# Performance work log

Hardware: AMD Instinct MI355X
Metric: run time of the kernel (lower is better)

## Reference

```python
import jax, jax.numpy as jnp
import numpy as np

B, I, J = 2, 2048, 2048
DIM = 1024
H = 16
DH = 64
INNER = H * DH
EPS = 1e-5


def _layernorm(x, g, b):
    mu = jnp.mean(x, axis=-1, keepdims=True)
    var = jnp.var(x, axis=-1, keepdims=True)
    return (x - mu) * jax.lax.rsqrt(var + EPS) * g + b


def setup_inputs() -> dict:
    key = jax.random.key(0)
    ks = jax.random.split(key, 12)
    s_in = 1.0 / np.sqrt(DIM)
    s_inner = 1.0 / np.sqrt(INNER)
    s_h = 1.0 / np.sqrt(H)
    return {
        "x": jax.random.normal(ks[0], (B, I, DIM), jnp.float32),
        "context": jax.random.normal(ks[1], (B, J, DIM), jnp.float32),
        "ln_g": jnp.ones((DIM,), jnp.float32),
        "ln_b": jnp.zeros((DIM,), jnp.float32),
        "ctx_ln_g": jnp.ones((DIM,), jnp.float32),
        "ctx_ln_b": jnp.zeros((DIM,), jnp.float32),
        "W_qk": jax.random.normal(ks[2], (DIM, INNER), jnp.float32) * s_in,
        "W_ctx_qk": jax.random.normal(ks[3], (DIM, INNER), jnp.float32) * s_in,
        "W_v": jax.random.normal(ks[4], (DIM, INNER), jnp.float32) * s_in,
        "W_ctx_v": jax.random.normal(ks[5], (DIM, INNER), jnp.float32) * s_in,
        "W_out": jax.random.normal(ks[6], (INNER, DIM), jnp.float32) * s_inner,
        "b_out": jnp.zeros((DIM,), jnp.float32),
        "W_ctx_out": jax.random.normal(ks[7], (INNER, DIM), jnp.float32) * s_inner,
        "b_ctx_out": jnp.zeros((DIM,), jnp.float32),
        "th_w": jax.random.normal(ks[8], (H, H), jnp.float32) * s_h,
        "ctx_th_w": jax.random.normal(ks[9], (H, H), jnp.float32) * s_h,
    }


def reference(x, context, ln_g, ln_b, ctx_ln_g, ctx_ln_b, W_qk, W_ctx_qk,
              W_v, W_ctx_v, W_out, b_out, W_ctx_out, b_ctx_out, th_w, ctx_th_w):
    b, i, j = x.shape[0], x.shape[1], context.shape[1]
    scale = DH ** -0.5
    xn = _layernorm(x, ln_g, ln_b)
    cn = _layernorm(context, ctx_ln_g, ctx_ln_b)

    def split_heads(t):  # [b, n, h*d] -> [b, h, n, d]
        return t.reshape(t.shape[0], t.shape[1], H, DH).transpose(0, 2, 1, 3)

    qk = split_heads(xn @ W_qk)            # [b, h, i, d]
    ctx_qk = split_heads(cn @ W_ctx_qk)    # [b, h, j, d]
    v = split_heads(xn @ W_v)              # [b, h, i, d]
    ctx_v = split_heads(cn @ W_ctx_v)      # [b, h, j, d]

    sim = jnp.einsum('bhid,bhjd->bhij', qk, ctx_qk) * scale  # shared sim matrix
    attn = jax.nn.softmax(sim, axis=-1)       # softmax over j
    ctx_attn = jax.nn.softmax(sim, axis=-2)   # softmax over i

    # talking heads: 1x1 conv over head dim
    attn = jnp.einsum('gh,bhij->bgij', th_w, attn)
    ctx_attn = jnp.einsum('gh,bhij->bgij', ctx_th_w, ctx_attn)

    out = jnp.einsum('bhij,bhjd->bhid', attn, ctx_v)       # [b, h, i, d]
    ctx_out = jnp.einsum('bhij,bhid->bhjd', ctx_attn, v)   # [b, h, j, d]

    def merge_heads(t):  # [b, h, n, d] -> [b, n, h*d]
        return t.transpose(0, 2, 1, 3).reshape(t.shape[0], t.shape[2], INNER)

    out = merge_heads(out) @ W_out + b_out
    ctx_out = merge_heads(ctx_out) @ W_ctx_out + b_ctx_out
    return out, ctx_out
```

## Files before the change

kernel.cpp:

```cpp
#include <hip/hip_runtime.h>
#include <hip/hip_bf16.h>
#include <cstdint>

#define DIM_   1024
#define H_     16
#define DH_    64
#define INNER_ 1024
#define B_     2
#define I_     2048
#define J_     2048
#define SCALE_ 0.125f

using bf16x8 = __attribute__((ext_vector_type(8))) short;
using f32x4  = __attribute__((ext_vector_type(4))) float;

__device__ __forceinline__ unsigned short f2bf(float f) {
  unsigned int u = __float_as_uint(f);
  u = (u + 0x7FFFu + ((u >> 16) & 1u)) >> 16;
  return (unsigned short)u;
}
__device__ __forceinline__ float bf2f(unsigned short h) {
  return __uint_as_float(((unsigned int)h) << 16);
}

__device__ __forceinline__ void gld16(const unsigned short* g, unsigned short* l) {
  __builtin_amdgcn_global_load_lds(
      (const __attribute__((address_space(1))) unsigned int*)g,
      (__attribute__((address_space(3))) unsigned int*)l, 16, 0, 0);
}

__global__ __launch_bounds__(256) void ln_cast_kernel(
    const float* __restrict__ in, const float* __restrict__ g,
    const float* __restrict__ bb, unsigned short* __restrict__ out) {
  int row = blockIdx.x;
  int t = threadIdx.x;
  const float4* rp = (const float4*)(in + (size_t)row * DIM_);
  float4 v = rp[t];
  float s  = v.x + v.y + v.z + v.w;
  float ss = v.x * v.x + v.y * v.y + v.z * v.z + v.w * v.w;
  for (int o = 1; o < 64; o <<= 1) {
    s  += __shfl_xor(s, o, 64);
    ss += __shfl_xor(ss, o, 64);
  }
  __shared__ float ls[4], lss[4];
  int wave = t >> 6, lane = t & 63;
  if (lane == 0) { ls[wave] = s; lss[wave] = ss; }
  __syncthreads();
  s  = ls[0] + ls[1] + ls[2] + ls[3];
  ss = lss[0] + lss[1] + lss[2] + lss[3];
  float mu  = s * (1.0f / DIM_);
  float var = ss * (1.0f / DIM_) - mu * mu;
  float rstd = rsqrtf(var + 1e-5f);
  float4 gv = ((const float4*)g)[t];
  float4 bv = ((const float4*)bb)[t];
  ushort4 o4;
  o4.x = f2bf((v.x - mu) * rstd * gv.x + bv.x);
  o4.y = f2bf((v.y - mu) * rstd * gv.y + bv.y);
  o4.z = f2bf((v.z - mu) * rstd * gv.z + bv.z);
  o4.w = f2bf((v.w - mu) * rstd * gv.w + bv.w);
  ((ushort4*)(out + (size_t)row * DIM_))[t] = o4;
}

__global__ __launch_bounds__(256) void transpose_cast_f32(
    const float* __restrict__ in, unsigned short* __restrict__ out, int R, int C) {
  __shared__ float tile[32][33];
  int z = blockIdx.z;
  const float* ip = in + (size_t)z * R * C;
  unsigned short* op = out + (size_t)z * R * C;
  int c0 = blockIdx.x * 32, r0 = blockIdx.y * 32;
  int tx = threadIdx.x, ty = threadIdx.y;
  for (int k = 0; k < 4; k++)
    tile[ty * 4 + k][tx] = ip[(size_t)(r0 + ty * 4 + k) * C + c0 + tx];
  __syncthreads();
  for (int k = 0; k < 4; k++)
    op[(size_t)(c0 + ty * 4 + k) * R + r0 + tx] = f2bf(tile[tx][ty * 4 + k]);
}

__global__ __launch_bounds__(256) void transpose_bf16(
    const unsigned short* __restrict__ in, unsigned short* __restrict__ out, int R, int C) {
  __shared__ unsigned short tile[32][33];
  int z = blockIdx.z;
  const unsigned short* ip = in + (size_t)z * R * C;
  unsigned short* op = out + (size_t)z * R * C;
  int c0 = blockIdx.x * 32, r0 = blockIdx.y * 32;
  int tx = threadIdx.x, ty = threadIdx.y;
  for (int k = 0; k < 4; k++)
    tile[ty * 4 + k][tx] = ip[(size_t)(r0 + ty * 4 + k) * C + c0 + tx];
  __syncthreads();
  for (int k = 0; k < 4; k++)
    op[(size_t)(c0 + ty * 4 + k) * R + r0 + tx] = tile[tx][ty * 4 + k];
}

__global__ __launch_bounds__(256) void gemm_qkv(
    const unsigned short* __restrict__ A0, const unsigned short* __restrict__ A1,
    const unsigned short* __restrict__ Bt0, const unsigned short* __restrict__ Bt1,
    unsigned short* __restrict__ qkO0, unsigned short* __restrict__ vO0,
    unsigned short* __restrict__ qkO1, unsigned short* __restrict__ vO1,
    int M, int K) {
  __shared__ unsigned short As[128 * 32];
  __shared__ unsigned short Bs[128 * 32];
  int z = blockIdx.z;
  const unsigned short* A  = z ? A1 : A0;
  const unsigned short* Bt = z ? Bt1 : Bt0;
  unsigned short* qkO = z ? qkO1 : qkO0;
  unsigned short* vO  = z ? vO1 : vO0;
  int t = threadIdx.x;
  int lane = t & 63, wave = t >> 6;
  int m0 = blockIdx.y * 128, n0 = blockIdx.x * 128;
  int wm = (wave >> 1) * 64, wn = (wave & 1) * 64;
  int l15 = lane & 15, lk = lane >> 4;
  int srow = t >> 2, scol = (t & 3) * 8;
  f32x4 acc[4][4] = {};

  for (int k0 = 0; k0 < K; k0 += 32) {
    gld16(&A[(size_t)(m0 + srow) * K + k0 + scol],       &As[wave * 512]);
    gld16(&A[(size_t)(m0 + srow + 64) * K + k0 + scol],  &As[2048 + wave * 512]);
    gld16(&Bt[(size_t)(n0 + srow) * K + k0 + scol],      &Bs[wave * 512]);
    gld16(&Bt[(size_t)(n0 + srow + 64) * K + k0 + scol], &Bs[2048 + wave * 512]);
    __syncthreads();
    bf16x8 af[4], bfr[4];
#pragma unroll
    for (int mi = 0; mi < 4; mi++) af[mi]  = *(const bf16x8*)&As[(wm + mi * 16 + l15) * 32 + lk * 8];
#pragma unroll
    for (int ni = 0; ni < 4; ni++) bfr[ni] = *(const bf16x8*)&Bs[(wn + ni * 16 + l15) * 32 + lk * 8];
#pragma unroll
    for (int mi = 0; mi < 4; mi++)
#pragma unroll
      for (int ni = 0; ni < 4; ni++)
        acc[mi][ni] = __builtin_amdgcn_mfma_f32_16x16x32_bf16(af[mi], bfr[ni], acc[mi][ni], 0, 0, 0);
    __syncthreads();
  }
  unsigned short* dst = (n0 < 1024) ? qkO : vO;
  int nbase = n0 & 1023;
#pragma unroll
  for (int mi = 0; mi < 4; mi++)
#pragma unroll
    for (int ni = 0; ni < 4; ni++) {
      int col = nbase + wn + ni * 16 + l15;
#pragma unroll
      for (int r = 0; r < 4; r++) {
        int row = m0 + wm + mi * 16 + lk * 4 + r;
        dst[(size_t)row * INNER_ + col] = f2bf(acc[mi][ni][r]);
      }
    }
}

__global__ __launch_bounds__(256) void gemm_out(
    const unsigned short* __restrict__ A0, const unsigned short* __restrict__ A1,
    const unsigned short* __restrict__ Bt0, const unsigned short* __restrict__ Bt1,
    const float* __restrict__ bias0, const float* __restrict__ bias1,
    float* __restrict__ C0, float* __restrict__ C1,
    int M, int N, int K) {
  __shared__ unsigned short As[128 * 32];
  __shared__ unsigned short Bs[128 * 32];
  int z = blockIdx.z;
  const unsigned short* A  = z ? A1 : A0;
  const unsigned short* Bt = z ? Bt1 : Bt0;
  const float* bias = z ? bias1 : bias0;
  float* Cout = z ? C1 : C0;
  int t = threadIdx.x;
  int lane = t & 63, wave = t >> 6;
  int m0 = blockIdx.y * 128, n0 = blockIdx.x * 128;
  int wm = (wave >> 1) * 64, wn = (wave & 1) * 64;
  int l15 = lane & 15, lk = lane >> 4;
  int srow = t >> 2, scol = (t & 3) * 8;
  f32x4 acc[4][4] = {};

  for (int k0 = 0; k0 < K; k0 += 32) {
    gld16(&A[(size_t)(m0 + srow) * K + k0 + scol],       &As[wave * 512]);
    gld16(&A[(size_t)(m0 + srow + 64) * K + k0 + scol],  &As[2048 + wave * 512]);
    gld16(&Bt[(size_t)(n0 + srow) * K + k0 + scol],      &Bs[wave * 512]);
    gld16(&Bt[(size_t)(n0 + srow + 64) * K + k0 + scol], &Bs[2048 + wave * 512]);
    __syncthreads();
    bf16x8 af[4], bfr[4];
#pragma unroll
    for (int mi = 0; mi < 4; mi++) af[mi]  = *(const bf16x8*)&As[(wm + mi * 16 + l15) * 32 + lk * 8];
#pragma unroll
    for (int ni = 0; ni < 4; ni++) bfr[ni] = *(const bf16x8*)&Bs[(wn + ni * 16 + l15) * 32 + lk * 8];
#pragma unroll
    for (int mi = 0; mi < 4; mi++)
#pragma unroll
      for (int ni = 0; ni < 4; ni++)
        acc[mi][ni] = __builtin_amdgcn_mfma_f32_16x16x32_bf16(af[mi], bfr[ni], acc[mi][ni], 0, 0, 0);
    __syncthreads();
  }
#pragma unroll
  for (int mi = 0; mi < 4; mi++)
#pragma unroll
    for (int ni = 0; ni < 4; ni++) {
      int col = n0 + wn + ni * 16 + l15;
      float bsv = bias[col];
#pragma unroll
      for (int r = 0; r < 4; r++) {
        int row = m0 + wm + mi * 16 + lk * 4 + r;
        Cout[(size_t)row * N + col] = acc[mi][ni][r] + bsv;
      }
    }
}

__global__ __launch_bounds__(256) void stats_kernel(
    const unsigned short* __restrict__ qk, const unsigned short* __restrict__ ck,
    float* __restrict__ rsum, float* __restrict__ csum, int NQ, int NK) {
  int zz = blockIdx.z;
  int b = zz & 1, dir = zz >> 1;
  const unsigned short* Q  = dir ? ck : qk;
  const unsigned short* Kc = dir ? qk : ck;
  float* out = dir ? csum : rsum;
  int h = blockIdx.y, i0 = blockIdx.x * 64;
  int t = threadIdx.x, lane = t & 63, wave = t >> 6;
  int l15 = lane & 15, lk = lane >> 4;
  const size_t qbase = ((size_t)b * NQ + i0) * INNER_ + h * DH_;
  bf16x8 af[4][2];
#pragma unroll
  for (int mi = 0; mi < 4; mi++)
#pragma unroll
    for (int ks = 0; ks < 2; ks++)
      af[mi][ks] = *(const bf16x8*)&Q[qbase + (size_t)(mi * 16 + l15) * INNER_ + ks * 32 + lk * 8];
  float racc[4][4] = {};
  for (int j0 = wave * 16; j0 < NK; j0 += 64) {
    const size_t kbase = ((size_t)b * NK + j0 + l15) * INNER_ + h * DH_ + lk * 8;
    bf16x8 b0 = *(const bf16x8*)&Kc[kbase];
    bf16x8 b1 = *(const bf16x8*)&Kc[kbase + 32];
#pragma unroll
    for (int mi = 0; mi < 4; mi++) {
      f32x4 acc = {};
      acc = __builtin_amdgcn_mfma_f32_16x16x32_bf16(af[mi][0], b0, acc, 0, 0, 0);
      acc = __builtin_amdgcn_mfma_f32_16x16x32_bf16(af[mi][1], b1, acc, 0, 0, 0);
#pragma unroll
      for (int r = 0; r < 4; r++) racc[mi][r] += __expf(acc[r] * SCALE_);
    }
  }
#pragma unroll
  for (int o = 1; o < 16; o <<= 1)
#pragma unroll
    for (int mi = 0; mi < 4; mi++)
#pragma unroll
      for (int r = 0; r < 4; r++) racc[mi][r] += __shfl_xor(racc[mi][r], o, 64);
  __shared__ float part[4][64];
  if (l15 == 0)
#pragma unroll
    for (int mi = 0; mi < 4; mi++)
#pragma unroll
      for (int r = 0; r < 4; r++) part[wave][mi * 16 + lk * 4 + r] = racc[mi][r];
  __syncthreads();
  if (t < 64)
    out[((size_t)b * H_ + h) * NQ + i0 + t] = part[0][t] + part[1][t] + part[2][t] + part[3][t];
}

#define MSROW 40
#define MSG   (32 * MSROW + 8)
__global__ __launch_bounds__(256, 2) void fused_attn_kernel(
    const unsigned short* __restrict__ Q, const unsigned short* __restrict__ Kc,
    const unsigned short* __restrict__ Vt, const float* __restrict__ rsum,
    const float* __restrict__ thw,
    float* __restrict__ p0, float* __restrict__ p1,
    float* __restrict__ p2, float* __restrict__ p3,
    int NQ, int NK, int CHUNK) {
  __shared__ unsigned short Pb[4 * 256 * 16];
  __shared__ unsigned short Ms[16 * MSG];
  __shared__ float lrS[512];
  int n = blockIdx.x;
  int combo = n & 7;
  int b = combo >> 2, jc = combo & 3;
  int i0 = (n >> 3) * 32;
  float* __restrict__ Op = (jc == 0) ? p0 : (jc == 1) ? p1 : (jc == 2) ? p2 : p3;
  int t = threadIdx.x, lane = t & 63, wave = t >> 6;
  int l15 = lane & 15, lk = lane >> 4;

  lrS[t]       = -__logf(rsum[((size_t)b * H_ + (t >> 5)) * NQ + i0 + (t & 31)]);
  lrS[t + 256] = -__logf(rsum[((size_t)b * H_ + ((t + 256) >> 5)) * NQ + i0 + (t & 31)]);

  bf16x8 tfrag;
  {
    int part = lk >> 1, hb = (lk & 1) * 8;
#pragma unroll
    for (int e = 0; e < 8; e++) {
      float a = thw[l15 * H_ + hb + e];
      unsigned short hi = f2bf(a);
      tfrag[e] = (short)(part == 0 ? hi : f2bf(a - bf2f(hi)));
    }
  }
  __syncthreads();

  bf16x8 qpre[4][2][2];
#pragma unroll
  for (int hh = 0; hh < 4; hh++)
#pragma unroll
    for (int is = 0; is < 2; is++)
#pragma unroll
      for (int kk = 0; kk < 2; kk++)
        qpre[hh][is][kk] = *(const bf16x8*)&Q[((size_t)b * NQ + i0 + is * 16 + l15) * INNER_
                                              + (wave * 4 + hh) * 64 + kk * 32 + lk * 8];

  f32x4 acc[32] = {};
  const int jbeg = jc * CHUNK;

  for (int js = 0; js < CHUNK; js += 32) {
    int j0 = jbeg + js;
    const unsigned short* Kb0 = Kc + ((size_t)b * NK + j0 + l15) * INNER_;
    const unsigned short* Kb1 = Kb0 + (size_t)16 * INNER_;
    unsigned int stage[2][2][4][2];
#pragma unroll
    for (int hh = 0; hh < 4; hh++) {
      int h = wave * 4 + hh;
      bf16x8 kb00 = *(const bf16x8*)&Kb0[h * 64 + lk * 8];
      bf16x8 kb01 = *(const bf16x8*)&Kb0[h * 64 + 32 + lk * 8];
      bf16x8 kb10 = *(const bf16x8*)&Kb1[h * 64 + lk * 8];
      bf16x8 kb11 = *(const bf16x8*)&Kb1[h * 64 + 32 + lk * 8];
#pragma unroll
      for (int is = 0; is < 2; is++) {
        f32x4 s0 = {}, s1 = {};
        s0 = __builtin_amdgcn_mfma_f32_16x16x32_bf16(qpre[hh][is][0], kb00, s0, 0, 0, 0);
        s0 = __builtin_amdgcn_mfma_f32_16x16x32_bf16(qpre[hh][is][1], kb01, s0, 0, 0, 0);
        s1 = __builtin_amdgcn_mfma_f32_16x16x32_bf16(qpre[hh][is][0], kb10, s1, 0, 0, 0);
        s1 = __builtin_amdgcn_mfma_f32_16x16x32_bf16(qpre[hh][is][1], kb11, s1, 0, 0, 0);
        f32x4 lr = *(const f32x4*)&lrS[h * 32 + is * 16 + lk * 4];
#pragma unroll
        for (int r = 0; r < 4; r++) {
          unsigned int b0 = f2bf(__expf(fmaf(s0[r], SCALE_, lr[r])));
          unsigned int b1 = f2bf(__expf(fmaf(s1[r], SCALE_, lr[r])));
          if (hh & 1) { stage[is][0][r][hh >> 1] |= b0 << 16; stage[is][1][r][hh >> 1] |= b1 << 16; }
          else        { stage[is][0][r][hh >> 1]  = b0;       stage[is][1][r][hh >> 1]  = b1; }
        }
      }
    }
#pragma unroll
    for (int is = 0; is < 2; is++)
#pragma unroll
      for (int jp = 0; jp < 2; jp++)
#pragma unroll
        for (int r = 0; r < 4; r++) {
          int row = (lk * 4 + r) * 16 + l15;
          int col = (wave * 4) ^ ((row & 1) << 3);
          uint2 u = { stage[is][jp][r][0], stage[is][jp][r][1] };
          *(uint2*)&Pb[(is + jp * 2) * 256 * 16 + row * 16 + col] = u;
        }
    __syncthreads();
    {
      int isub = wave & 1, jstrip = wave >> 1;
      const unsigned short* pr = &Pb[(isub + jstrip * 2) * 256 * 16];
#pragma unroll
      for (int p = 0; p < 16; p++) {
        int row = p * 16 + l15;
        int col = ((lk & 1) << 3) ^ ((row & 1) << 3);
        bf16x8 af = *(const bf16x8*)&pr[row * 16 + col];
        f32x4 m = {};
        m = __builtin_amdgcn_mfma_f32_16x16x32_bf16(af, tfrag, m, 0, 0, 0);
        ushort4 o;
        o.x = f2bf(m[0]); o.y = f2bf(m[1]); o.z = f2bf(m[2]); o.w = f2bf(m[3]);
        *(ushort4*)&Ms[l15 * MSG + (isub * 16 + p) * MSROW + jstrip * 16 + lk * 4] = o;
      }
    }
    __syncthreads();
#pragma unroll
    for (int gi = 0; gi < 4; gi++) {
      int g = wave * 4 + gi;
      bf16x8 ma0 = *(const bf16x8*)&Ms[g * MSG + l15 * MSROW + lk * 8];
      bf16x8 ma1 = *(const bf16x8*)&Ms[g * MSG + (16 + l15) * MSROW + lk * 8];
#pragma unroll
      for (int nt = 0; nt < 4; nt++) {
        const size_t vb = ((size_t)b * INNER_ + g * 64 + nt * 16 + l15) * NK + j0 + lk * 8;
        bf16x8 v0 = *(const bf16x8*)&Vt[vb];
        acc[gi * 8 + nt]     = __builtin_amdgcn_mfma_f32_16x16x32_bf16(ma0, v0, acc[gi * 8 + nt], 0, 0, 0);
        acc[gi * 8 + 4 + nt] = __builtin_amdgcn_mfma_f32_16x16x32_bf16(ma1, v0, acc[gi * 8 + 4 + nt], 0, 0, 0);
      }
    }
  }
#pragma unroll
  for (int gi = 0; gi < 4; gi++)
#pragma unroll
    for (int is = 0; is < 2; is++)
#pragma unroll
      for (int nt = 0; nt < 4; nt++) {
        int col = (wave * 4 + gi) * 64 + nt * 16 + l15;
#pragma unroll
        for (int r = 0; r < 4; r++)
          Op[((size_t)b * NQ + i0 + is * 16 + lk * 4 + r) * INNER_ + col] = acc[gi * 8 + is * 4 + nt][r];
      }
}

__global__ __launch_bounds__(256) void reduce_cast_kernel(
    const float* __restrict__ p0, const float* __restrict__ p1,
    const float* __restrict__ p2, const float* __restrict__ p3,
    unsigned short* __restrict__ out, int n4) {
  int idx = blockIdx.x * 256 + threadIdx.x;
  if (idx >= n4) return;
  float4 v = ((const float4*)p0)[idx];
  float4 w = ((const float4*)p1)[idx];
  float4 a = ((const float4*)p2)[idx];
  float4 c = ((const float4*)p3)[idx];
  v.x += w.x + a.x + c.x; v.y += w.y + a.y + c.y;
  v.z += w.z + a.z + c.z; v.w += w.w + a.w + c.w;
  ushort4 o;
  o.x = f2bf(v.x); o.y = f2bf(v.y); o.z = f2bf(v.z); o.w = f2bf(v.w);
  ((ushort4*)out)[idx] = o;
}

extern "C" void kernel_launch(void* const* d_in, const int* in_sizes, int n_in,
                              void* d_out, int out_size, void* d_ws, size_t ws_size,
                              hipStream_t stream) {
  const float* x      = (const float*)d_in[0];
  const float* ctx    = (const float*)d_in[1];
  const float* ln_g   = (const float*)d_in[2];
  const float* ln_b   = (const float*)d_in[3];
  const float* cln_g  = (const float*)d_in[4];
  const float* cln_b  = (const float*)d_in[5];
  const float* W_qk   = (const float*)d_in[6];
  const float* W_cqk  = (const float*)d_in[7];
  const float* W_v    = (const float*)d_in[8];
  const float* W_cv   = (const float*)d_in[9];
  const float* W_out  = (const float*)d_in[10];
  const float* b_out  = (const float*)d_in[11];
  const float* W_cout = (const float*)d_in[12];
  const float* b_cout = (const float*)d_in[13];
  const float* th_w   = (const float*)d_in[14];
  const float* cth_w  = (const float*)d_in[15];

  char* w = (char*)d_ws;
  const size_t SZ_ROW = (size_t)B_ * I_ * DIM_ * 2;
  const size_t SZ_W   = (size_t)DIM_ * INNER_ * 2;
  unsigned short* xn    = (unsigned short*)w; w += SZ_ROW;
  unsigned short* cn    = (unsigned short*)w; w += SZ_ROW;
  unsigned short* WqvX  = (unsigned short*)w; w += 2 * SZ_W;
  unsigned short* WqvC  = (unsigned short*)w; w += 2 * SZ_W;
  unsigned short* Woutt = (unsigned short*)w; w += SZ_W;
  unsigned short* Wcoutt= (unsigned short*)w; w += SZ_W;
  unsigned short* qk    = (unsigned short*)w; w += SZ_ROW;
  unsigned short* ck    = (unsigned short*)w; w += SZ_ROW;
  unsigned short* vv    = (unsigned short*)w; w += SZ_ROW;
  unsigned short* cv    = (unsigned short*)w; w += SZ_ROW;
  unsigned short* vT    = (unsigned short*)w; w += SZ_ROW;
  unsigned short* cvT   = (unsigned short*)w; w += SZ_ROW;
  float* rsum = (float*)w; w += (size_t)B_ * H_ * I_ * 4;
  float* csum = (float*)w; w += (size_t)B_ * H_ * J_ * 4;
  unsigned short* Oh1 = (unsigned short*)w; w += SZ_ROW;
  unsigned short* Oh2 = (unsigned short*)w; w += SZ_ROW;

  const size_t PART = (size_t)B_ * I_ * INNER_ * 4;
  float* p0 = (float*)xn;
  float* p1 = (float*)vv;
  float* p2 = (float*)w;
  float* p3 = (float*)(w + PART);

  dim3 tb(32, 8);
  ln_cast_kernel<<<B_ * I_, 256, 0, stream>>>(x, ln_g, ln_b, xn);
  ln_cast_kernel<<<B_ * J_, 256, 0, stream>>>(ctx, cln_g, cln_b, cn);

  const size_t WOFF = (size_t)DIM_ * INNER_;
  transpose_cast_f32<<<dim3(32, 32, 1), tb, 0, stream>>>(W_qk,   WqvX,        DIM_, INNER_);
  transpose_cast_f32<<<dim3(32, 32, 1), tb, 0, stream>>>(W_v,    WqvX + WOFF, DIM_, INNER_);
  transpose_cast_f32<<<dim3(32, 32, 1), tb, 0, stream>>>(W_cqk,  WqvC,        DIM_, INNER_);
  transpose_cast_f32<<<dim3(32, 32, 1), tb, 0, stream>>>(W_cv,   WqvC + WOFF, DIM_, INNER_);
  transpose_cast_f32<<<dim3(32, 32, 1), tb, 0, stream>>>(W_out,  Woutt, INNER_, DIM_);
  transpose_cast_f32<<<dim3(32, 32, 1), tb, 0, stream>>>(W_cout, Wcoutt,INNER_, DIM_);

  gemm_qkv<<<dim3(2 * INNER_ / 128, (B_ * I_) / 128, 2), 256, 0, stream>>>(
      xn, cn, WqvX, WqvC, qk, vv, ck, cv, B_ * I_, DIM_);

  transpose_bf16<<<dim3(INNER_ / 32, I_ / 32, B_), tb, 0, stream>>>(vv, vT, I_, INNER_);
  transpose_bf16<<<dim3(INNER_ / 32, J_ / 32, B_), tb, 0, stream>>>(cv, cvT, J_, INNER_);

  stats_kernel<<<dim3(I_ / 64, H_, 4), 256, 0, stream>>>(qk, ck, rsum, csum, I_, J_);

  const int n4 = (B_ * I_ * INNER_) / 4;
  fused_attn_kernel<<<(I_ / 32) * 4 * B_, 256, 0, stream>>>(
      qk, ck, cvT, rsum, th_w, p0, p1, p2, p3, I_, J_, J_ / 4);
  reduce_cast_kernel<<<n4 / 256, 256, 0, stream>>>(p0, p1, p2, p3, Oh1, n4);
  fused_attn_kernel<<<(J_ / 32) * 4 * B_, 256, 0, stream>>>(
      ck, qk, vT, csum, cth_w, p0, p1, p2, p3, J_, I_, I_ / 4);
  reduce_cast_kernel<<<n4 / 256, 256, 0, stream>>>(p0, p1, p2, p3, Oh2, n4);

  gemm_out<<<dim3(DIM_ / 128, (B_ * I_) / 128, 2), 256, 0, stream>>>(
      Oh1, Oh2, Woutt, Wcoutt, b_out, b_cout,
      (float*)d_out, ((float*)d_out) + (size_t)B_ * I_ * DIM_,
      B_ * I_, DIM_, INNER_);
}
```

Measured before the change: 782.2 us.

## Split fused attention across eight waves with two heads each

The fused attention kernel now launches with 512 threads (eight waves), and each wave handles two heads instead of four. This halves per-wave accumulators and Q fragments, which reduces register pressure and should allow more waves in flight. The second head's Q fragments are loaded inside the loop instead of held in registers, and the LDS P buffer uses a new XOR swizzle with 32-bit stores and loads. In exchange the kernel issues more LDS transactions and reloads Q each iteration, and more waves contend at each barrier.

```diff
diff --git a/kernel.cpp b/kernel.cpp
--- a/kernel.cpp
+++ b/kernel.cpp
@@ -249,7 +249,7 @@
 
 #define MSROW 40
 #define MSG   (32 * MSROW + 8)
-__global__ __launch_bounds__(256, 2) void fused_attn_kernel(
+__global__ __launch_bounds__(512, 4) void fused_attn_kernel(
     const unsigned short* __restrict__ Q, const unsigned short* __restrict__ Kc,
     const unsigned short* __restrict__ Vt, const float* __restrict__ rsum,
     const float* __restrict__ thw,
@@ -267,8 +267,7 @@
   int t = threadIdx.x, lane = t & 63, wave = t >> 6;
   int l15 = lane & 15, lk = lane >> 4;
 
-  lrS[t]       = -__logf(rsum[((size_t)b * H_ + (t >> 5)) * NQ + i0 + (t & 31)]);
-  lrS[t + 256] = -__logf(rsum[((size_t)b * H_ + ((t + 256) >> 5)) * NQ + i0 + (t & 31)]);
+  lrS[t] = -__logf(rsum[((size_t)b * H_ + (t >> 5)) * NQ + i0 + (t & 31)]);
 
   bf16x8 tfrag;
   {
@@ -282,45 +281,56 @@
   }
   __syncthreads();
 
-  bf16x8 qpre[4][2][2];
-#pragma unroll
-  for (int hh = 0; hh < 4; hh++)
-#pragma unroll
-    for (int is = 0; is < 2; is++)
-#pragma unroll
-      for (int kk = 0; kk < 2; kk++)
-        qpre[hh][is][kk] = *(const bf16x8*)&Q[((size_t)b * NQ + i0 + is * 16 + l15) * INNER_
-                                              + (wave * 4 + hh) * 64 + kk * 32 + lk * 8];
-
-  f32x4 acc[32] = {};
+  const unsigned short* Qrow = Q + ((size_t)b * NQ + i0 + l15) * INNER_;
+  bf16x8 qpre[2][2];
+#pragma unroll
+  for (int is = 0; is < 2; is++)
+#pragma unroll
+    for (int kk = 0; kk < 2; kk++)
+      qpre[is][kk] = *(const bf16x8*)&Qrow[(size_t)(is * 16) * INNER_
+                                           + (wave * 2) * 64 + kk * 32 + lk * 8];
+
+  int xsw2 = (((l15 >> 2) & 3) << 1) | (lk & 1);
+  int colw = (wave * 2) ^ (xsw2 << 1);
+
+  f32x4 acc[16] = {};
   const int jbeg = jc * CHUNK;
 
   for (int js = 0; js < CHUNK; js += 32) {
     int j0 = jbeg + js;
     const unsigned short* Kb0 = Kc + ((size_t)b * NK + j0 + l15) * INNER_;
-    const unsigned short* Kb1 = Kb0 + (size_t)16 * INNER_;
-    unsigned int stage[2][2][4][2];
-#pragma unroll
-    for (int hh = 0; hh < 4; hh++) {
-      int h = wave * 4 + hh;
-      bf16x8 kb00 = *(const bf16x8*)&Kb0[h * 64 + lk * 8];
-      bf16x8 kb01 = *(const bf16x8*)&Kb0[h * 64 + 32 + lk * 8];
-      bf16x8 kb10 = *(const bf16x8*)&Kb1[h * 64 + lk * 8];
-      bf16x8 kb11 = *(const bf16x8*)&Kb1[h * 64 + 32 + lk * 8];
-#pragma unroll
-      for (int is = 0; is < 2; is++) {
-        f32x4 s0 = {}, s1 = {};
-        s0 = __builtin_amdgcn_mfma_f32_16x16x32_bf16(qpre[hh][is][0], kb00, s0, 0, 0, 0);
-        s0 = __builtin_amdgcn_mfma_f32_16x16x32_bf16(qpre[hh][is][1], kb01, s0, 0, 0, 0);
-        s1 = __builtin_amdgcn_mfma_f32_16x16x32_bf16(qpre[hh][is][0], kb10, s1, 0, 0, 0);
-        s1 = __builtin_amdgcn_mfma_f32_16x16x32_bf16(qpre[hh][is][1], kb11, s1, 0, 0, 0);
-        f32x4 lr = *(const f32x4*)&lrS[h * 32 + is * 16 + lk * 4];
-#pragma unroll
-        for (int r = 0; r < 4; r++) {
-          unsigned int b0 = f2bf(__expf(fmaf(s0[r], SCALE_, lr[r])));
-          unsigned int b1 = f2bf(__expf(fmaf(s1[r], SCALE_, lr[r])));
-          if (hh & 1) { stage[is][0][r][hh >> 1] |= b0 << 16; stage[is][1][r][hh >> 1] |= b1 << 16; }
-          else        { stage[is][0][r][hh >> 1]  = b0;       stage[is][1][r][hh >> 1]  = b1; }
+    unsigned int stage[2][2][4];
+#pragma unroll
+    for (int hh = 0; hh < 2; hh++) {
+      int h = wave * 2 + hh;
+      bf16x8 q1[2][2];
+      if (hh == 1) {
+#pragma unroll
+        for (int is = 0; is < 2; is++)
+#pragma unroll
+          for (int kk = 0; kk < 2; kk++)
+            q1[is][kk] = *(const bf16x8*)&Qrow[(size_t)(is * 16) * INNER_
+                                               + h * 64 + kk * 32 + lk * 8];
+      }
+#pragma unroll
+      for (int jp = 0; jp < 2; jp++) {
+        const unsigned short* Kb = Kb0 + (size_t)(jp * 16) * INNER_;
+        bf16x8 kb0 = *(const bf16x8*)&Kb[h * 64 + lk * 8];
+        bf16x8 kb1 = *(const bf16x8*)&Kb[h * 64 + 32 + lk * 8];
+#pragma unroll
+        for (int is = 0; is < 2; is++) {
+          bf16x8 a0 = hh ? q1[is][0] : qpre[is][0];
+          bf16x8 a1 = hh ? q1[is][1] : qpre[is][1];
+          f32x4 s = {};
+          s = __builtin_amdgcn_mfma_f32_16x16x32_bf16(a0, kb0, s, 0, 0, 0);
+          s = __builtin_amdgcn_mfma_f32_16x16x32_bf16(a1, kb1, s, 0, 0, 0);
+          f32x4 lr = *(const f32x4*)&lrS[h * 32 + is * 16 + lk * 4];
+#pragma unroll
+          for (int r = 0; r < 4; r++) {
+            unsigned int bv = f2bf(__expf(fmaf(s[r], SCALE_, lr[r])));
+            if (hh) stage[is][jp][r] |= bv << 16;
+            else    stage[is][jp][r]  = bv;
+          }
         }
       }
     }
@@ -331,21 +341,27 @@
 #pragma unroll
         for (int r = 0; r < 4; r++) {
           int row = (lk * 4 + r) * 16 + l15;
-          int col = (wave * 4) ^ ((row & 1) << 3);
-          uint2 u = { stage[is][jp][r][0], stage[is][jp][r][1] };
-          *(uint2*)&Pb[(is + jp * 2) * 256 * 16 + row * 16 + col] = u;
+          *(unsigned int*)&Pb[(is + jp * 2) * 4096 + row * 16 + colw] = stage[is][jp][r];
         }
     __syncthreads();
     {
-      int isub = wave & 1, jstrip = wave >> 1;
-      const unsigned short* pr = &Pb[(isub + jstrip * 2) * 256 * 16];
-#pragma unroll
-      for (int p = 0; p < 16; p++) {
+      int q = wave & 3, pbase = (wave >> 2) * 8;
+      int isub = q & 1, jstrip = q >> 1;
+      const unsigned short* pr = &Pb[q * 4096];
+      int cb = (lk & 1) << 3;
+      int xme = ((l15 >> 2) & 3) << 2;
+#pragma unroll
+      for (int p8 = 0; p8 < 8; p8++) {
+        int p = pbase + p8;
         int row = p * 16 + l15;
-        int col = ((lk & 1) << 3) ^ ((row & 1) << 3);
-        bf16x8 af = *(const bf16x8*)&pr[row * 16 + col];
+        int xr = xme | (((p >> 2) & 1) << 1);
+        union { bf16x8 v; unsigned int u[4]; } U;
+        U.u[0] = *(const unsigned int*)&pr[row * 16 + ((cb | 0) ^ xr)];
+        U.u[1] = *(const unsigned int*)&pr[row * 16 + ((cb | 2) ^ xr)];
+        U.u[2] = *(const unsigned int*)&pr[row * 16 + ((cb | 4) ^ xr)];
+        U.u[3] = *(const unsigned int*)&pr[row * 16 + ((cb | 6) ^ xr)];
         f32x4 m = {};
-        m = __builtin_amdgcn_mfma_f32_16x16x32_bf16(af, tfrag, m, 0, 0, 0);
+        m = __builtin_amdgcn_mfma_f32_16x16x32_bf16(U.v, tfrag, m, 0, 0, 0);
         ushort4 o;
         o.x = f2bf(m[0]); o.y = f2bf(m[1]); o.z = f2bf(m[2]); o.w = f2bf(m[3]);
         *(ushort4*)&Ms[l15 * MSG + (isub * 16 + p) * MSROW + jstrip * 16 + lk * 4] = o;
@@ -353,8 +369,8 @@
     }
     __syncthreads();
 #pragma unroll
-    for (int gi = 0; gi < 4; gi++) {
-      int g = wave * 4 + gi;
+    for (int gi = 0; gi < 2; gi++) {
+      int g = wave * 2 + gi;
       bf16x8 ma0 = *(const bf16x8*)&Ms[g * MSG + l15 * MSROW + lk * 8];
       bf16x8 ma1 = *(const bf16x8*)&Ms[g * MSG + (16 + l15) * MSROW + lk * 8];
 #pragma unroll
@@ -367,12 +383,12 @@
     }
   }
 #pragma unroll
-  for (int gi = 0; gi < 4; gi++)
+  for (int gi = 0; gi < 2; gi++)
 #pragma unroll
     for (int is = 0; is < 2; is++)
 #pragma unroll
       for (int nt = 0; nt < 4; nt++) {
-        int col = (wave * 4 + gi) * 64 + nt * 16 + l15;
+        int col = (wave * 2 + gi) * 64 + nt * 16 + l15;
 #pragma unroll
         for (int r = 0; r < 4; r++)
           Op[((size_t)b * NQ + i0 + is * 16 + lk * 4 + r) * INNER_ + col] = acc[gi * 8 + is * 4 + nt][r];
@@ -463,10 +479,10 @@
   stats_kernel<<<dim3(I_ / 64, H_, 4), 256, 0, stream>>>(qk, ck, rsum, csum, I_, J_);
 
   const int n4 = (B_ * I_ * INNER_) / 4;
-  fused_attn_kernel<<<(I_ / 32) * 4 * B_, 256, 0, stream>>>(
+  fused_attn_kernel<<<(I_ / 32) * 4 * B_, 512, 0, stream>>>(
       qk, ck, cvT, rsum, th_w, p0, p1, p2, p3, I_, J_, J_ / 4);
   reduce_cast_kernel<<<n4 / 256, 256, 0, stream>>>(p0, p1, p2, p3, Oh1, n4);
-  fused_attn_kernel<<<(J_ / 32) * 4 * B_, 256, 0, stream>>>(
+  fused_attn_kernel<<<(J_ / 32) * 4 * B_, 512, 0, stream>>>(
       ck, qk, vT, csum, cth_w, p0, p1, p2, p3, J_, I_, I_ / 4);
   reduce_cast_kernel<<<n4 / 256, 256, 0, stream>>>(p0, p1, p2, p3, Oh2, n4);
 
```

Result: slower. 949.1 us (+21.3%).
